# Kernel tuning notes

Hardware: AMD Instinct MI355X
Metric: run time of the kernel (lower is better)

The kernel has to match this reference:

```python
import jax, jax.numpy as jnp
import numpy as np

N_NODES = 50000
N_EDGES = 400000
HID = 256
NUM_LAYERS = 2
NUM_LEVELS = 8  # depth of the constructed leveled DAG


def _build_dag_edges():
    # Leveled DAG: NUM_LEVELS levels of equal size; every edge goes from
    # level l (src) to level l+1 (dst), guaranteeing termination in
    # exactly NUM_LEVELS topological sweeps.
    rng = np.random.default_rng(0)
    per_level = N_NODES // NUM_LEVELS
    dst_level = rng.integers(1, NUM_LEVELS, size=N_EDGES)
    dst = dst_level * per_level + rng.integers(0, per_level, size=N_EDGES)
    src = (dst_level - 1) * per_level + rng.integers(0, per_level, size=N_EDGES)
    return jnp.asarray(np.stack([src, dst]).astype(np.int32))


def setup_inputs() -> dict:
    key = jax.random.key(0)
    ks = jax.random.split(key, 8)
    s = 0.05
    V = jax.random.normal(ks[0], (N_NODES, HID), dtype=jnp.float32)
    E = _build_dag_edges()
    dense_w = jax.random.normal(ks[1], (HID, HID), dtype=jnp.float32) * s
    dense_b = jax.random.normal(ks[2], (HID,), dtype=jnp.float32) * s
    gru_w_ih = jax.random.normal(ks[3], (NUM_LAYERS, 3 * HID, HID), dtype=jnp.float32) * s
    gru_w_hh = jax.random.normal(ks[4], (NUM_LAYERS, 3 * HID, HID), dtype=jnp.float32) * s
    gru_b_ih = jax.random.normal(ks[5], (NUM_LAYERS, 3 * HID), dtype=jnp.float32) * s
    gru_b_hh = jax.random.normal(ks[6], (NUM_LAYERS, 3 * HID), dtype=jnp.float32) * s
    return {"V": V, "E": E, "dense_w": dense_w, "dense_b": dense_b,
            "gru_w_ih": gru_w_ih, "gru_w_hh": gru_w_hh,
            "gru_b_ih": gru_b_ih, "gru_b_hh": gru_b_hh}


def _gru_cell(x, h, w_ih, w_hh, b_ih, b_hh):
    gi = x @ w_ih.T + b_ih
    gh = h @ w_hh.T + b_hh
    i_r, i_z, i_n = jnp.split(gi, 3, axis=-1)
    h_r, h_z, h_n = jnp.split(gh, 3, axis=-1)
    r = jax.nn.sigmoid(i_r + h_r)
    z = jax.nn.sigmoid(i_z + h_z)
    n = jnp.tanh(i_n + r * h_n)
    return (1.0 - z) * n + z * h


def _dag_gru_layer(x, src, dst, w_ih, w_hh, b_ih, b_hh):
    N = x.shape[0]
    H = w_hh.shape[1]

    def step(carry, _):
        hidden, avail = carry
        # nodes that are dst of an edge whose source is still available
        blocked = jnp.zeros((N,), dtype=bool).at[dst].max(avail[src])
        leaf = avail & ~blocked
        use = leaf[dst]  # edges feeding a leaf node this sweep
        msgs = jnp.where(use[:, None], hidden[src], 0.0)  # [E, H]
        agg = jax.ops.segment_sum(msgs, dst, num_segments=N)  # [N, H]
        new_h = _gru_cell(x, agg, w_ih, w_hh, b_ih, b_hh)
        hidden = jnp.where(leaf[:, None], new_h, hidden)
        return (hidden, avail & ~leaf), None

    init = (jnp.zeros((N, H), dtype=x.dtype), jnp.ones((N,), dtype=bool))
    (hidden, _), _ = jax.lax.scan(step, init, None, length=NUM_LEVELS)
    return hidden


def reference(V, E, dense_w, dense_b, gru_w_ih, gru_w_hh, gru_b_ih, gru_b_hh):
    src, dst = E[0], E[1]
    hidden = V @ dense_w.T + dense_b
    for l in range(NUM_LAYERS):
        hidden = _dag_gru_layer(hidden, src, dst,
                                gru_w_ih[l], gru_w_hh[l],
                                gru_b_ih[l], gru_b_hh[l])
    return hidden
```

## Files before the change

### kernel.cpp

```cpp
#include <hip/hip_runtime.h>

#define HID 256
#define NSTEPS 8

typedef __attribute__((ext_vector_type(4))) float f32x4;
typedef __attribute__((ext_vector_type(8))) short s16x8;
typedef __attribute__((ext_vector_type(4))) short s16x4;

__device__ __forceinline__ unsigned short f2bf(float f) {
  unsigned u = __builtin_bit_cast(unsigned, f);
  u += 0x7fffu + ((u >> 16) & 1u);
  return (unsigned short)(u >> 16);
}
__device__ __forceinline__ float bf2f(unsigned short s) {
  return __builtin_bit_cast(float, ((unsigned)s) << 16);
}

__device__ __forceinline__ f32x4 mfma16(s16x8 a, s16x8 b, f32x4 c) {
  return __builtin_amdgcn_mfma_f32_16x16x32_bf16(a, b, c, 0, 0, 0);
}

__device__ __forceinline__ void split3(const float* p, s16x8& a0, s16x8& a1, s16x8& a2) {
  f32x4 u = *(const f32x4*)p;
  f32x4 v = *(const f32x4*)(p + 4);
  float f[8] = {u[0], u[1], u[2], u[3], v[0], v[1], v[2], v[3]};
#pragma unroll
  for (int j = 0; j < 8; ++j) {
    unsigned short l0 = f2bf(f[j]);
    float r1 = f[j] - bf2f(l0);
    unsigned short l1 = f2bf(r1);
    float r2 = r1 - bf2f(l1);
    a0[j] = (short)l0;
    a1[j] = (short)l1;
    a2[j] = (short)f2bf(r2);
  }
}


__global__ void k_limb(const float* __restrict__ in, short* __restrict__ o0,
                       short* __restrict__ o1, short* __restrict__ o2, int n) {
  int i = blockIdx.x * 256 + threadIdx.x;
  if (i < n) {
    float x = in[i];
    unsigned short l0 = f2bf(x);
    float r1 = x - bf2f(l0);
    unsigned short l1 = f2bf(r1);
    o0[i] = (short)l0;
    o1[i] = (short)l1;
    o2[i] = (short)f2bf(r1 - bf2f(l1));
  }
}


__global__ void k_indeg(const int* __restrict__ dst, int* __restrict__ indeg, int E) {
  int e = blockIdx.x * blockDim.x + threadIdx.x;
  if (e < E) atomicAdd(&indeg[dst[e]], 1);
}

__global__ void k_blocksum(const int* __restrict__ indeg, int* __restrict__ bsum, int N) {
  __shared__ int s[256];
  int i = blockIdx.x * 256 + threadIdx.x;
  s[threadIdx.x] = (i < N) ? indeg[i] : 0;
  __syncthreads();
  for (int st = 128; st > 0; st >>= 1) {
    if (threadIdx.x < st) s[threadIdx.x] += s[threadIdx.x + st];
    __syncthreads();
  }
  if (threadIdx.x == 0) bsum[blockIdx.x] = s[0];
}

__global__ void k_bscan(const int* __restrict__ bsum, int* __restrict__ boff,
                        int NB, int* __restrict__ total) {
  if (threadIdx.x == 0 && blockIdx.x == 0) {
    int a = 0;
    for (int i = 0; i < NB; ++i) { boff[i] = a; a += bsum[i]; }
    *total = a;
  }
}

__global__ void k_scan3(const int* __restrict__ indeg, const int* __restrict__ boff,
                        int* __restrict__ csr_off, int N) {
  __shared__ int s[256];
  int tx = threadIdx.x;
  int i = blockIdx.x * 256 + tx;
  int v = (i < N) ? indeg[i] : 0;
  s[tx] = v;
  __syncthreads();
  for (int st = 1; st < 256; st <<= 1) {
    int t = (tx >= st) ? s[tx - st] : 0;
    __syncthreads();
    s[tx] += t;
    __syncthreads();
  }
  if (i < N) csr_off[i] = boff[blockIdx.x] + s[tx] - v;
}

__global__ void k_fill(const int* __restrict__ src, const int* __restrict__ dst,
                       const int* __restrict__ csr_off, int* __restrict__ cursor,
                       int* __restrict__ csr_src, int E) {
  int e = blockIdx.x * blockDim.x + threadIdx.x;
  if (e < E) {
    int d = dst[e];
    int p = atomicAdd(&cursor[d], 1);
    csr_src[csr_off[d] + p] = src[e];
  }
}


__global__ void k_aggf2(const float* __restrict__ HA, const float* __restrict__ HB,
                        int t, int PB,
                        const int* __restrict__ csr_off, const int* __restrict__ csr_src,
                        float* __restrict__ aggFA, float* __restrict__ aggFB,
                        short* __restrict__ GA0, short* __restrict__ GA1,
                        short* __restrict__ GA2,
                        short* __restrict__ GB0, short* __restrict__ GB1,
                        short* __restrict__ GB2) {
  const int z = blockIdx.z;
  const int s = t - z;
  if (s < 0 || s >= NSTEPS) return;
  const float* H = z ? HB : HA;
  float* aggF = z ? aggFB : aggFA;
  short* G0 = z ? GB0 : GA0;
  short* G1 = z ? GB1 : GA1;
  short* G2 = z ? GB2 : GA2;

  const int grp = threadIdx.x >> 6, lane = threadIdx.x & 63;
  const int r = blockIdx.x * 4 + grp;
  if (r >= PB) return;
  const int node = s * PB + r;
  const int b = csr_off[node], e = csr_off[node + 1];
  const int c4 = lane * 4;
  f32x4 acc = (f32x4){0.f, 0.f, 0.f, 0.f};
  for (int j = b; j < e; ++j) {
    f32x4 v = *(const f32x4*)&H[(size_t)csr_src[j] * HID + c4];
    acc[0] += v[0]; acc[1] += v[1]; acc[2] += v[2]; acc[3] += v[3];
  }
  size_t o = (size_t)r * HID + c4;
  *(f32x4*)&aggF[o] = acc;
  s16x4 g0, g1, g2;
#pragma unroll
  for (int q = 0; q < 4; ++q) {
    unsigned short l0 = f2bf(acc[q]);
    float r1 = acc[q] - bf2f(l0);
    unsigned short l1 = f2bf(r1);
    g0[q] = (short)l0;
    g1[q] = (short)l1;
    g2[q] = (short)f2bf(r1 - bf2f(l1));
  }
  *(s16x4*)&G0[o] = g0;
  *(s16x4*)&G1[o] = g1;
  *(s16x4*)&G2[o] = g2;
}

__global__ __launch_bounds__(256, 2)
void k_dense8(const float* __restrict__ V, const short* __restrict__ dwS,
              const float* __restrict__ db,
              short* __restrict__ A0, short* __restrict__ A1,
              short* __restrict__ A2, int M) {
  __shared__ s16x8 lds[2][24 * 64];
  const int tid = threadIdx.x;
  const int w = tid >> 6, lane = tid & 63;
  const int lr = lane & 15, lg = lane >> 4;
  const int c0 = blockIdx.x * 128;
  const int m0 = blockIdx.y * 64 + w * 16;
  const float* xrow = V + (size_t)min(m0 + lr, M - 1) * HID;

  const short* sp[6];
  int so[6];
#pragma unroll
  for (int q = 0; q < 6; ++q) {
    int f = w * 6 + q;
    int a = f >> 3, t = f & 7;
    sp[q] = dwS + a * (HID * HID) + (size_t)(c0 + t * 16 + lr) * HID + lg * 8;
    so[q] = f * 64 + lane;
  }

  s16x8 rr[6];
#pragma unroll
  for (int q = 0; q < 6; ++q) rr[q] = *(const s16x8*)(sp[q]);
#pragma unroll
  for (int q = 0; q < 6; ++q) lds[0][so[q]] = rr[q];

  f32x4 acc[8];
#pragma unroll
  for (int t = 0; t < 8; ++t) acc[t] = (f32x4){0.f, 0.f, 0.f, 0.f};

  for (int kc = 0; kc < 8; ++kc) {
    if (kc < 7) {
#pragma unroll
      for (int q = 0; q < 6; ++q) rr[q] = *(const s16x8*)(sp[q] + (kc + 1) * 32);
    }
    __syncthreads();
    const s16x8* buf = lds[kc & 1];
    int kb = kc * 32 + lg * 8;
    s16x8 x0, x1, x2;
    split3(xrow + kb, x0, x1, x2);
#pragma unroll
    for (int t = 0; t < 8; ++t) {
      s16x8 w0f = buf[(0 * 8 + t) * 64 + lane];
      s16x8 w1f = buf[(1 * 8 + t) * 64 + lane];
      s16x8 w2f = buf[(2 * 8 + t) * 64 + lane];
      f32x4 a = acc[t];
      a = mfma16(x0, w0f, a);
      a = mfma16(x0, w1f, a);
      a = mfma16(x1, w0f, a);
      a = mfma16(x1, w1f, a);
      a = mfma16(x0, w2f, a);
      a = mfma16(x2, w0f, a);
      acc[t] = a;
    }
    if (kc < 7) {
#pragma unroll
      for (int q = 0; q < 6; ++q) lds[(kc + 1) & 1][so[q]] = rr[q];
    }
  }

#pragma unroll
  for (int t = 0; t < 8; ++t) {
    int col = c0 + t * 16 + lr;
    float bb = db[col];
#pragma unroll
    for (int r = 0; r < 4; ++r) {
      int row = m0 + lg * 4 + r;
      if (row < M) {
        float v = acc[t][r] + bb;
        unsigned short l0 = f2bf(v);
        float r1 = v - bf2f(l0);
        unsigned short l1 = f2bf(r1);
        size_t o = (size_t)row * HID + col;
        A0[o] = (short)l0;
        A1[o] = (short)l1;
        A2[o] = (short)f2bf(r1 - bf2f(l1));
      }
    }
  }
}

__global__ __launch_bounds__(256, 2)
void k_step2(const short* __restrict__ A0, const short* __restrict__ A1,
             const short* __restrict__ A2,
             const short* __restrict__ B0, const short* __restrict__ B1,
             const short* __restrict__ B2,
             const short* __restrict__ GA0, const short* __restrict__ GA1,
             const short* __restrict__ GA2,
             const short* __restrict__ GB0, const short* __restrict__ GB1,
             const short* __restrict__ GB2,
             const float* __restrict__ aggFA, const float* __restrict__ aggFB,
             const short* __restrict__ wS,
             const float* __restrict__ b_ih, const float* __restrict__ b_hh,
             int t, int PB, float* __restrict__ Bfp, float* __restrict__ outp) {
  const int z = blockIdx.z;
  const int s = t - z;
  if (s < 0 || s >= NSTEPS) return;

  const short* X0 = z ? B0 : A0;
  const short* X1 = z ? B1 : A1;
  const short* X2 = z ? B2 : A2;
  const short* G0 = z ? GB0 : GA0;
  const short* G1 = z ? GB1 : GA1;
  const short* G2 = z ? GB2 : GA2;
  const float* aggF = z ? aggFB : aggFA;
  const int AS = 768 * HID;
  const short* wSL = wS + (size_t)z * 6 * AS;
  const float* bi = b_ih + z * 768;
  const float* bh = b_hh + z * 768;
  float* Hf = z ? outp : Bfp;
  const bool outl = (z == 0);

  __shared__ s16x8 lds[2][36 * 64];
  const int tid = threadIdx.x;
  const int w = tid >> 6, lane = tid & 63;
  const int lr = lane & 15, lg = lane >> 4;
  const int c0 = blockIdx.x * 32;
  const int m0w = blockIdx.y * 128 + w * 32;
  const int nb = s * PB;

  const short* sp[9];
  int so[9];
#pragma unroll
  for (int q = 0; q < 9; ++q) {
    int f = w * 9 + q;
    int a = f / 6, gt = f - a * 6, g = gt >> 1, tt = gt & 1;
    sp[q] = wSL + (size_t)a * AS + (size_t)(g * HID + c0 + tt * 16 + lr) * HID + lg * 8;
    so[q] = f * 64 + lane;
  }

  s16x8 rr[9];
#pragma unroll
  for (int q = 0; q < 9; ++q) rr[q] = *(const s16x8*)(sp[q]);
#pragma unroll
  for (int q = 0; q < 9; ++q) lds[0][so[q]] = rr[q];

  f32x4 acci[3][2][2], acch[3][2][2];
#pragma unroll
  for (int g = 0; g < 3; ++g)
#pragma unroll
    for (int tt = 0; tt < 2; ++tt)
#pragma unroll
      for (int rg = 0; rg < 2; ++rg) {
        acci[g][tt][rg] = (f32x4){0.f, 0.f, 0.f, 0.f};
        acch[g][tt][rg] = (f32x4){0.f, 0.f, 0.f, 0.f};
      }

  int rowA[2];
  rowA[0] = min(m0w + lr, PB - 1);
  rowA[1] = min(m0w + 16 + lr, PB - 1);

  for (int kc = 0; kc < 8; ++kc) {
    if (kc < 7) {
#pragma unroll
      for (int q = 0; q < 9; ++q) rr[q] = *(const s16x8*)(sp[q] + (kc + 1) * 32);
    }
    __syncthreads();
    const s16x8* buf = lds[kc & 1];
    const int kb = kc * 32 + lg * 8;
    s16x8 x0[2], x1[2], x2[2], g0[2], g1[2], g2[2];
#pragma unroll
    for (int rg = 0; rg < 2; ++rg) {
      size_t xb = (size_t)(nb + rowA[rg]) * HID + kb;
      x0[rg] = *(const s16x8*)&X0[xb];
      x1[rg] = *(const s16x8*)&X1[xb];
      x2[rg] = *(const s16x8*)&X2[xb];
      size_t gb = (size_t)rowA[rg] * HID + kb;
      g0[rg] = *(const s16x8*)&G0[gb];
      g1[rg] = *(const s16x8*)&G1[gb];
      g2[rg] = *(const s16x8*)&G2[gb];
    }
#pragma unroll
    for (int g = 0; g < 3; ++g) {
#pragma unroll
      for (int tt = 0; tt < 2; ++tt) {
        s16x8 wi0f = buf[(0 * 6 + g * 2 + tt) * 64 + lane];
        s16x8 wi1f = buf[(1 * 6 + g * 2 + tt) * 64 + lane];
        s16x8 wi2f = buf[(2 * 6 + g * 2 + tt) * 64 + lane];
        s16x8 wh0f = buf[(3 * 6 + g * 2 + tt) * 64 + lane];
        s16x8 wh1f = buf[(4 * 6 + g * 2 + tt) * 64 + lane];
        s16x8 wh2f = buf[(5 * 6 + g * 2 + tt) * 64 + lane];
#pragma unroll
        for (int rg = 0; rg < 2; ++rg) {
          f32x4 a = acci[g][tt][rg];
          a = mfma16(x0[rg], wi0f, a);
          a = mfma16(x0[rg], wi1f, a);
          a = mfma16(x1[rg], wi0f, a);
          a = mfma16(x1[rg], wi1f, a);
          a = mfma16(x0[rg], wi2f, a);
          a = mfma16(x2[rg], wi0f, a);
          acci[g][tt][rg] = a;
          f32x4 h = acch[g][tt][rg];
          h = mfma16(g0[rg], wh0f, h);
          h = mfma16(g0[rg], wh1f, h);
          h = mfma16(g1[rg], wh0f, h);
          h = mfma16(g1[rg], wh1f, h);
          h = mfma16(g0[rg], wh2f, h);
          h = mfma16(g2[rg], wh0f, h);
          acch[g][tt][rg] = h;
        }
      }
    }
    if (kc < 7) {
#pragma unroll
      for (int q = 0; q < 9; ++q) lds[(kc + 1) & 1][so[q]] = rr[q];
    }
  }

#pragma unroll
  for (int tt = 0; tt < 2; ++tt) {
    int col = c0 + tt * 16 + lr;
    float bir = bi[col], biz = bi[HID + col], bin = bi[2 * HID + col];
    float bhr = bh[col], bhz = bh[HID + col], bhn = bh[2 * HID + col];
#pragma unroll
    for (int rg = 0; rg < 2; ++rg) {
#pragma unroll
      for (int r = 0; r < 4; ++r) {
        int row = m0w + rg * 16 + lg * 4 + r;
        if (row < PB) {
          float ir = acci[0][tt][rg][r] + bir;
          float iz = acci[1][tt][rg][r] + biz;
          float in_ = acci[2][tt][rg][r] + bin;
          float hr = acch[0][tt][rg][r] + bhr;
          float hz = acch[1][tt][rg][r] + bhz;
          float hn = acch[2][tt][rg][r] + bhn;
          float rgate = 1.f / (1.f + expf(-(ir + hr)));
          float zg = 1.f / (1.f + expf(-(iz + hz)));
          float ng = tanhf(in_ + rgate * hn);
          float a = aggF[(size_t)row * HID + col];
          float h = (1.f - zg) * ng + zg * a;
          size_t o = (size_t)(nb + row) * HID + col;
          Hf[o] = h;
          if (outl) {
            unsigned short l0 = f2bf(h);
            float r1 = h - bf2f(l0);
            unsigned short l1 = f2bf(r1);
            ((short*)B0)[o] = (short)l0;
            ((short*)B1)[o] = (short)l1;
            ((short*)B2)[o] = (short)f2bf(r1 - bf2f(l1));
          }
        }
      }
    }
  }
}


extern "C" void kernel_launch(void* const* d_in, const int* in_sizes, int n_in,
                              void* d_out, int out_size, void* d_ws, size_t ws_size,
                              hipStream_t stream) {
  const float* V = (const float*)d_in[0];
  const int* E = (const int*)d_in[1];
  const float* dense_w = (const float*)d_in[2];
  const float* dense_b = (const float*)d_in[3];
  const float* w_ih = (const float*)d_in[4];
  const float* w_hh = (const float*)d_in[5];
  const float* b_ih = (const float*)d_in[6];
  const float* b_hh = (const float*)d_in[7];
  const int N = in_sizes[0] / HID;
  const int Ecnt = in_sizes[1] / 2;
  const int PB = N / NSTEPS;
  const int* src = E;
  const int* dst = E + Ecnt;
  float* out = (float*)d_out;

  const size_t AS = (size_t)768 * HID;

  char* p = (char*)d_ws;
  short* A0 = (short*)p;    p += (size_t)N * HID * 2;
  short* A1 = (short*)p;    p += (size_t)N * HID * 2;
  short* A2 = (short*)p;    p += (size_t)N * HID * 2;
  float* B = (float*)p;     p += (size_t)N * HID * 4;
  short* B0 = (short*)p;    p += (size_t)N * HID * 2;
  short* B1 = (short*)p;    p += (size_t)N * HID * 2;
  short* B2 = (short*)p;    p += (size_t)N * HID * 2;
  float* aggFA = (float*)p; p += (size_t)PB * HID * 4;
  float* aggFB = (float*)p; p += (size_t)PB * HID * 4;
  short* GA0 = (short*)p;   p += (size_t)PB * HID * 2;
  short* GA1 = (short*)p;   p += (size_t)PB * HID * 2;
  short* GA2 = (short*)p;   p += (size_t)PB * HID * 2;
  short* GB0 = (short*)p;   p += (size_t)PB * HID * 2;
  short* GB1 = (short*)p;   p += (size_t)PB * HID * 2;
  short* GB2 = (short*)p;   p += (size_t)PB * HID * 2;
  short* dwS = (short*)p;   p += (size_t)3 * HID * HID * 2;
  short* wS = (short*)p;    p += (size_t)2 * 6 * AS * 2;
  int* indeg = (int*)p;     p += (size_t)N * 4;
  int* cursor = (int*)p;    p += (size_t)N * 4;
  int* csr_off = (int*)p;   p += (size_t)(N + 1) * 4;
  int* csr_src = (int*)p;   p += (size_t)Ecnt * 4;
  int* bsum = (int*)p;      p += 256 * 4;
  int* boff = (int*)p;      p += 256 * 4;

  hipMemsetAsync(indeg, 0, (size_t)2 * N * 4, stream);

  const int TB = 256;
  const int egrid = (Ecnt + TB - 1) / TB;
  const int NB = (N + 255) / 256;
  const int wgrid = ((int)AS + 255) / 256;

  k_limb<<<(HID * HID + 255) / 256, TB, 0, stream>>>(
      dense_w, dwS, dwS + HID * HID, dwS + 2 * HID * HID, HID * HID);
  for (int l = 0; l < 2; ++l) {
    k_limb<<<wgrid, TB, 0, stream>>>(w_ih + l * AS, wS + (l * 6 + 0) * AS,
                                     wS + (l * 6 + 1) * AS, wS + (l * 6 + 2) * AS, (int)AS);
    k_limb<<<wgrid, TB, 0, stream>>>(w_hh + l * AS, wS + (l * 6 + 3) * AS,
                                     wS + (l * 6 + 4) * AS, wS + (l * 6 + 5) * AS, (int)AS);
  }

  k_dense8<<<dim3(2, (N + 63) / 64), TB, 0, stream>>>(V, dwS, dense_b, A0, A1, A2, N);

  k_indeg<<<egrid, TB, 0, stream>>>(dst, indeg, Ecnt);
  k_blocksum<<<NB, TB, 0, stream>>>(indeg, bsum, N);
  k_bscan<<<1, 1, 0, stream>>>(bsum, boff, NB, csr_off + N);
  k_scan3<<<NB, TB, 0, stream>>>(indeg, boff, csr_off, N);
  k_fill<<<egrid, TB, 0, stream>>>(src, dst, csr_off, cursor, csr_src, Ecnt);

  const dim3 agrid((PB + 3) / 4, 1, 2);
  const dim3 sgrid(HID / 32, (PB + 127) / 128, 2);
  for (int t = 0; t <= NSTEPS; ++t) {
    k_aggf2<<<agrid, TB, 0, stream>>>(B, out, t, PB, csr_off, csr_src,
                                      aggFA, aggFB, GA0, GA1, GA2, GB0, GB1, GB2);
    k_step2<<<sgrid, TB, 0, stream>>>(A0, A1, A2, B0, B1, B2,
                                      GA0, GA1, GA2, GB0, GB1, GB2,
                                      aggFA, aggFB, wS, b_ih, b_hh,
                                      t, PB, B, out);
  }
}
```

Baseline: 1.358 ms.

## Make GRU step kernel persistent with full-K weight slice resident in LDS

The per-step GRU kernel now uses 512-thread blocks, each owning a 16-column output slice. Each block loads all split-bf16 weights for that slice across the full K dimension into LDS once, then loops over row tiles in a grid-stride fashion. The launch grid becomes fixed (16x8x2) instead of scaling with the number of rows. This removes repeated weight streaming and per-k-chunk barriers, at the cost of large LDS use (about 147KB), fewer blocks in flight, and halving the columns per wave, which lowers reuse of the activation loads.

```diff
diff --git a/kernel.cpp b/kernel.cpp
--- a/kernel.cpp
+++ b/kernel.cpp
@@ -236,8 +236,8 @@
   }
 }
 
-__global__ __launch_bounds__(256, 2)
-void k_step2(const short* __restrict__ A0, const short* __restrict__ A1,
+__global__ __launch_bounds__(512, 2)
+void k_stepP(const short* __restrict__ A0, const short* __restrict__ A1,
              const short* __restrict__ A2,
              const short* __restrict__ B0, const short* __restrict__ B1,
              const short* __restrict__ B2,
@@ -267,133 +267,111 @@
   float* Hf = z ? outp : Bfp;
   const bool outl = (z == 0);
 
-  __shared__ s16x8 lds[2][36 * 64];
+  __shared__ s16x8 lds[8][18][64];
   const int tid = threadIdx.x;
   const int w = tid >> 6, lane = tid & 63;
   const int lr = lane & 15, lg = lane >> 4;
-  const int c0 = blockIdx.x * 32;
-  const int m0w = blockIdx.y * 128 + w * 32;
+  const int c0 = blockIdx.x * 16;
   const int nb = s * PB;
 
-  const short* sp[9];
-  int so[9];
-#pragma unroll
-  for (int q = 0; q < 9; ++q) {
-    int f = w * 9 + q;
-    int a = f / 6, gt = f - a * 6, g = gt >> 1, tt = gt & 1;
-    sp[q] = wSL + (size_t)a * AS + (size_t)(g * HID + c0 + tt * 16 + lr) * HID + lg * 8;
-    so[q] = f * 64 + lane;
-  }
-
-  s16x8 rr[9];
-#pragma unroll
-  for (int q = 0; q < 9; ++q) rr[q] = *(const s16x8*)(sp[q]);
-#pragma unroll
-  for (int q = 0; q < 9; ++q) lds[0][so[q]] = rr[q];
-
-  f32x4 acci[3][2][2], acch[3][2][2];
-#pragma unroll
-  for (int g = 0; g < 3; ++g)
-#pragma unroll
-    for (int tt = 0; tt < 2; ++tt)
+  for (int u = w; u < 144; u += 8) {
+    int f = u >> 3, kc = u & 7;
+    int a = f / 3, g = f - a * 3;
+    const short* srcp = wSL + (size_t)a * AS + (size_t)(g * HID + c0 + lr) * HID + kc * 32 + lg * 8;
+    lds[kc][f][lane] = *(const s16x8*)srcp;
+  }
+  __syncthreads();
+
+  for (int m0b = blockIdx.y * 256; m0b < PB; m0b += 256 * gridDim.y) {
+    const int m0w = m0b + w * 32;
+    int rowA[2];
+    rowA[0] = min(m0w + lr, PB - 1);
+    rowA[1] = min(m0w + 16 + lr, PB - 1);
+
+    f32x4 acci[3][2], acch[3][2];
+#pragma unroll
+    for (int g = 0; g < 3; ++g)
 #pragma unroll
       for (int rg = 0; rg < 2; ++rg) {
-        acci[g][tt][rg] = (f32x4){0.f, 0.f, 0.f, 0.f};
-        acch[g][tt][rg] = (f32x4){0.f, 0.f, 0.f, 0.f};
+        acci[g][rg] = (f32x4){0.f, 0.f, 0.f, 0.f};
+        acch[g][rg] = (f32x4){0.f, 0.f, 0.f, 0.f};
       }
 
-  int rowA[2];
-  rowA[0] = min(m0w + lr, PB - 1);
-  rowA[1] = min(m0w + 16 + lr, PB - 1);
-
-  for (int kc = 0; kc < 8; ++kc) {
-    if (kc < 7) {
-#pragma unroll
-      for (int q = 0; q < 9; ++q) rr[q] = *(const s16x8*)(sp[q] + (kc + 1) * 32);
-    }
-    __syncthreads();
-    const s16x8* buf = lds[kc & 1];
-    const int kb = kc * 32 + lg * 8;
-    s16x8 x0[2], x1[2], x2[2], g0[2], g1[2], g2[2];
-#pragma unroll
-    for (int rg = 0; rg < 2; ++rg) {
-      size_t xb = (size_t)(nb + rowA[rg]) * HID + kb;
-      x0[rg] = *(const s16x8*)&X0[xb];
-      x1[rg] = *(const s16x8*)&X1[xb];
-      x2[rg] = *(const s16x8*)&X2[xb];
-      size_t gb = (size_t)rowA[rg] * HID + kb;
-      g0[rg] = *(const s16x8*)&G0[gb];
-      g1[rg] = *(const s16x8*)&G1[gb];
-      g2[rg] = *(const s16x8*)&G2[gb];
-    }
-#pragma unroll
-    for (int g = 0; g < 3; ++g) {
-#pragma unroll
-      for (int tt = 0; tt < 2; ++tt) {
-        s16x8 wi0f = buf[(0 * 6 + g * 2 + tt) * 64 + lane];
-        s16x8 wi1f = buf[(1 * 6 + g * 2 + tt) * 64 + lane];
-        s16x8 wi2f = buf[(2 * 6 + g * 2 + tt) * 64 + lane];
-        s16x8 wh0f = buf[(3 * 6 + g * 2 + tt) * 64 + lane];
-        s16x8 wh1f = buf[(4 * 6 + g * 2 + tt) * 64 + lane];
-        s16x8 wh2f = buf[(5 * 6 + g * 2 + tt) * 64 + lane];
+    for (int kc = 0; kc < 8; ++kc) {
+      const int kb = kc * 32 + lg * 8;
+      s16x8 x0[2], x1[2], x2[2], g0[2], g1[2], g2[2];
+#pragma unroll
+      for (int rg = 0; rg < 2; ++rg) {
+        size_t xb = (size_t)(nb + rowA[rg]) * HID + kb;
+        x0[rg] = *(const s16x8*)&X0[xb];
+        x1[rg] = *(const s16x8*)&X1[xb];
+        x2[rg] = *(const s16x8*)&X2[xb];
+        size_t gb = (size_t)rowA[rg] * HID + kb;
+        g0[rg] = *(const s16x8*)&G0[gb];
+        g1[rg] = *(const s16x8*)&G1[gb];
+        g2[rg] = *(const s16x8*)&G2[gb];
+      }
+#pragma unroll
+      for (int g = 0; g < 3; ++g) {
+        s16x8 wi0f = lds[kc][0 * 3 + g][lane];
+        s16x8 wi1f = lds[kc][1 * 3 + g][lane];
+        s16x8 wi2f = lds[kc][2 * 3 + g][lane];
+        s16x8 wh0f = lds[kc][3 * 3 + g][lane];
+        s16x8 wh1f = lds[kc][4 * 3 + g][lane];
+        s16x8 wh2f = lds[kc][5 * 3 + g][lane];
 #pragma unroll
         for (int rg = 0; rg < 2; ++rg) {
-          f32x4 a = acci[g][tt][rg];
+          f32x4 a = acci[g][rg];
           a = mfma16(x0[rg], wi0f, a);
           a = mfma16(x0[rg], wi1f, a);
           a = mfma16(x1[rg], wi0f, a);
           a = mfma16(x1[rg], wi1f, a);
           a = mfma16(x0[rg], wi2f, a);
           a = mfma16(x2[rg], wi0f, a);
-          acci[g][tt][rg] = a;
-          f32x4 h = acch[g][tt][rg];
+          acci[g][rg] = a;
+          f32x4 h = acch[g][rg];
           h = mfma16(g0[rg], wh0f, h);
           h = mfma16(g0[rg], wh1f, h);
           h = mfma16(g1[rg], wh0f, h);
           h = mfma16(g1[rg], wh1f, h);
           h = mfma16(g0[rg], wh2f, h);
           h = mfma16(g2[rg], wh0f, h);
-          acch[g][tt][rg] = h;
+          acch[g][rg] = h;
         }
       }
     }
-    if (kc < 7) {
-#pragma unroll
-      for (int q = 0; q < 9; ++q) lds[(kc + 1) & 1][so[q]] = rr[q];
-    }
-  }
-
-#pragma unroll
-  for (int tt = 0; tt < 2; ++tt) {
-    int col = c0 + tt * 16 + lr;
-    float bir = bi[col], biz = bi[HID + col], bin = bi[2 * HID + col];
-    float bhr = bh[col], bhz = bh[HID + col], bhn = bh[2 * HID + col];
-#pragma unroll
-    for (int rg = 0; rg < 2; ++rg) {
-#pragma unroll
-      for (int r = 0; r < 4; ++r) {
-        int row = m0w + rg * 16 + lg * 4 + r;
-        if (row < PB) {
-          float ir = acci[0][tt][rg][r] + bir;
-          float iz = acci[1][tt][rg][r] + biz;
-          float in_ = acci[2][tt][rg][r] + bin;
-          float hr = acch[0][tt][rg][r] + bhr;
-          float hz = acch[1][tt][rg][r] + bhz;
-          float hn = acch[2][tt][rg][r] + bhn;
-          float rgate = 1.f / (1.f + expf(-(ir + hr)));
-          float zg = 1.f / (1.f + expf(-(iz + hz)));
-          float ng = tanhf(in_ + rgate * hn);
-          float a = aggF[(size_t)row * HID + col];
-          float h = (1.f - zg) * ng + zg * a;
-          size_t o = (size_t)(nb + row) * HID + col;
-          Hf[o] = h;
-          if (outl) {
-            unsigned short l0 = f2bf(h);
-            float r1 = h - bf2f(l0);
-            unsigned short l1 = f2bf(r1);
-            ((short*)B0)[o] = (short)l0;
-            ((short*)B1)[o] = (short)l1;
-            ((short*)B2)[o] = (short)f2bf(r1 - bf2f(l1));
+
+    {
+      int col = c0 + lr;
+      float bir = bi[col], biz = bi[HID + col], bin = bi[2 * HID + col];
+      float bhr = bh[col], bhz = bh[HID + col], bhn = bh[2 * HID + col];
+#pragma unroll
+      for (int rg = 0; rg < 2; ++rg) {
+#pragma unroll
+        for (int r = 0; r < 4; ++r) {
+          int row = m0w + rg * 16 + lg * 4 + r;
+          if (row < PB) {
+            float ir = acci[0][rg][r] + bir;
+            float iz = acci[1][rg][r] + biz;
+            float in_ = acci[2][rg][r] + bin;
+            float hr = acch[0][rg][r] + bhr;
+            float hz = acch[1][rg][r] + bhz;
+            float hn = acch[2][rg][r] + bhn;
+            float rgate = 1.f / (1.f + expf(-(ir + hr)));
+            float zg = 1.f / (1.f + expf(-(iz + hz)));
+            float ng = tanhf(in_ + rgate * hn);
+            float a = aggF[(size_t)row * HID + col];
+            float h = (1.f - zg) * ng + zg * a;
+            size_t o = (size_t)(nb + row) * HID + col;
+            Hf[o] = h;
+            if (outl) {
+              unsigned short l0 = f2bf(h);
+              float r1 = h - bf2f(l0);
+              unsigned short l1 = f2bf(r1);
+              ((short*)B0)[o] = (short)l0;
+              ((short*)B1)[o] = (short)l1;
+              ((short*)B2)[o] = (short)f2bf(r1 - bf2f(l1));
+            }
           }
         }
       }
@@ -472,13 +450,13 @@
   k_fill<<<egrid, TB, 0, stream>>>(src, dst, csr_off, cursor, csr_src, Ecnt);
 
   const dim3 agrid((PB + 3) / 4, 1, 2);
-  const dim3 sgrid(HID / 32, (PB + 127) / 128, 2);
+  const dim3 sgrid(HID / 16, 8, 2);
   for (int t = 0; t <= NSTEPS; ++t) {
     k_aggf2<<<agrid, TB, 0, stream>>>(B, out, t, PB, csr_off, csr_src,
                                       aggFA, aggFB, GA0, GA1, GA2, GB0, GB1, GB2);
-    k_step2<<<sgrid, TB, 0, stream>>>(A0, A1, A2, B0, B1, B2,
-                                      GA0, GA1, GA2, GB0, GB1, GB2,
-                                      aggFA, aggFB, wS, b_ih, b_hh,
-                                      t, PB, B, out);
-  }
-}
+    k_stepP<<<sgrid, 512, 0, stream>>>(A0, A1, A2, B0, B1, B2,
+                                       GA0, GA1, GA2, GB0, GB1, GB2,
+                                       aggFA, aggFB, wS, b_ih, b_hh,
+                                       t, PB, B, out);
+  }
+}
```

After: 1.272 ms. 6.3% less time.
